# Optimization experiments

Hardware: AMD Instinct MI355X
Metric: run time of the kernel (lower is better)

The kernel has to match this reference:

```python
import jax, jax.numpy as jnp
import numpy as np

B = 4096
N_DENSE = 13
N_SPARSE = 26
VOCAB = 100000
EMB = 8
CIN_SIZE = [26, 128, 128]


def setup_inputs() -> dict:
    key = jax.random.key(0)
    ks = jax.random.split(key, 24)
    s = 0.05
    dense = jax.random.normal(ks[0], (B, N_DENSE), dtype=jnp.float32)
    sparse = jax.random.randint(ks[1], (B, N_SPARSE), 0, VOCAB).astype(jnp.float32)
    inputs = jnp.concatenate([dense, sparse], axis=1)  # [B, 39]
    emb_tables = jax.random.normal(ks[2], (N_SPARSE, VOCAB, EMB), dtype=jnp.float32) * s
    linear_W = jax.random.normal(ks[3], (39, 1), dtype=jnp.float32) * s
    linear_b = jnp.zeros((1,), dtype=jnp.float32)
    # CIN Conv3d weights: kernel (H_prev, H0, 1) with out_channels H_next -> [H_next, H_prev, H0]
    W_cin0 = jax.random.normal(ks[4], (CIN_SIZE[1], CIN_SIZE[0], CIN_SIZE[0]), dtype=jnp.float32) * s
    b_cin0 = jnp.zeros((CIN_SIZE[1],), dtype=jnp.float32)
    W_cin1 = jax.random.normal(ks[5], (CIN_SIZE[2], CIN_SIZE[1], CIN_SIZE[0]), dtype=jnp.float32) * s
    b_cin1 = jnp.zeros((CIN_SIZE[2],), dtype=jnp.float32)
    cin_lin_W = jax.random.normal(ks[6], (256, 1), dtype=jnp.float32) * s
    cin_lin_b = jnp.zeros((1,), dtype=jnp.float32)
    d_W1 = jax.random.normal(ks[7], (221, 256), dtype=jnp.float32) * s
    d_b1 = jnp.zeros((256,), dtype=jnp.float32)
    d_W2 = jax.random.normal(ks[8], (256, 128), dtype=jnp.float32) * s
    d_b2 = jnp.zeros((128,), dtype=jnp.float32)
    d_W3 = jax.random.normal(ks[9], (128, 64), dtype=jnp.float32) * s
    d_b3 = jnp.zeros((64,), dtype=jnp.float32)
    d_W4 = jax.random.normal(ks[10], (64, 1), dtype=jnp.float32) * s
    d_b4 = jnp.zeros((1,), dtype=jnp.float32)
    return dict(inputs=inputs, emb_tables=emb_tables, linear_W=linear_W, linear_b=linear_b,
                W_cin0=W_cin0, b_cin0=b_cin0, W_cin1=W_cin1, b_cin1=b_cin1,
                cin_lin_W=cin_lin_W, cin_lin_b=cin_lin_b,
                d_W1=d_W1, d_b1=d_b1, d_W2=d_W2, d_b2=d_b2,
                d_W3=d_W3, d_b3=d_b3, d_W4=d_W4, d_b4=d_b4)


def reference(inputs, emb_tables, linear_W, linear_b,
              W_cin0, b_cin0, W_cin1, b_cin1, cin_lin_W, cin_lin_b,
              d_W1, d_b1, d_W2, d_b2, d_W3, d_b3, d_W4, d_b4):
    dense_in = inputs[:, :N_DENSE]                       # [B, 13]
    sparse_idx = inputs[:, N_DENSE:].astype(jnp.int32)   # [B, 26]

    # linear part over the raw inputs
    linear_out = inputs @ linear_W + linear_b            # [B, 1]

    # per-field embedding lookup: tables [F, V, E], idx [B, F] -> emb [B, F, E]
    emb = jax.vmap(lambda t, i: t[i], in_axes=(0, 1), out_axes=1)(emb_tables, sparse_idx)

    # CIN: each layer is an outer product over fields followed by a full-extent
    # Conv3d, i.e. X_{l+1}[b,o,k] = sum_{i,j} X_l[b,i,k] * X_0[b,j,k] * W[o,i,j] + b[o]
    X0 = emb
    Xi = emb
    res = []
    for W, b in ((W_cin0, b_cin0), (W_cin1, b_cin1)):
        Xi = jnp.einsum('bik,bjk,oij->bok', Xi, X0, W) + b[None, :, None]
        res.append(Xi)
    cin_feat = jnp.sum(jnp.concatenate(res, axis=1), axis=-1)  # [B, 256]
    cin_out = jax.nn.relu(cin_feat @ cin_lin_W + cin_lin_b)    # [B, 1]

    # dense MLP over [dense | flattened embeddings]
    h = jnp.concatenate([dense_in, emb.reshape(emb.shape[0], -1)], axis=1)  # [B, 221]
    h = jax.nn.relu(h @ d_W1 + d_b1)
    h = jax.nn.relu(h @ d_W2 + d_b2)
    h = jax.nn.relu(h @ d_W3 + d_b3)
    dense_out = jax.nn.relu(h @ d_W4 + d_b4)                   # [B, 1]

    return jax.nn.sigmoid(linear_out + cin_out + dense_out).reshape(-1)  # [B]
```

## Files before the change

kernel.cpp:

```cpp
#include <hip/hip_runtime.h>
#include <math.h>

#define B     4096
#define ND    13
#define NS    26
#define NF    39
#define VOCAB 100000
#define NP    351
#define NPP   360
#define CHP   45
#define GSTR  28
#define RPB   4
#define XSS   212

#define OFF_GST 0
#define OFF_CST 10080
#define OFF_C2J 10088

__global__ __launch_bounds__(256) void k_pre(const float* __restrict__ W0,
                                             const float* __restrict__ W1,
                                             const float* __restrict__ b0,
                                             const float* __restrict__ b1,
                                             const float* __restrict__ clw,
                                             float* __restrict__ Gst,
                                             float* __restrict__ cst,
                                             float* __restrict__ c2j) {
    int blk = blockIdx.x, tid = threadIdx.x;
    if (blk < 26) {
        int j = blk;
        __shared__ float vh[2][128];
        __shared__ float vj[128];
        __shared__ float c2r[2];
        {
            int i = tid & 127, h = tid >> 7;
            const float* wp = W1 + (long)(h * 64) * 3328 + i * 26 + j;
            float acc = 0.f;
#pragma unroll 8
            for (int o = 0; o < 64; o++) acc += clw[128 + h * 64 + o] * wp[o * 3328];
            vh[h][i] = acc;
        }
        __syncthreads();
        if (tid < 128) {
            float vv = vh[0][tid] + vh[1][tid];
            vj[tid] = vv;
            float c = vv * b0[tid];
            for (int off = 32; off; off >>= 1) c += __shfl_down(c, off, 64);
            if ((tid & 63) == 0) c2r[tid >> 6] = c;
        }
        __syncthreads();
        if (tid == 0) c2j[j] = c2r[0] + c2r[1];
        for (int p = tid; p < NPP; p += 256) {
            float g = 0.f;
            if (p < NP) {
                int l = 0, rem = p;
                while (rem >= NS - l) { rem -= NS - l; l++; }
                int m = l + rem;
                float sym = (l != m) ? 1.f : 0.f;
                const float* wa = W0 + l * 26 + m;
                const float* wb = W0 + m * 26 + l;
#pragma unroll 8
                for (int i = 0; i < 128; i++)
                    g += vj[i] * (wa[i * 676] + sym * wb[i * 676]);
            }
            Gst[p * GSTR + j] = g;
        }
    } else if (blk == 26) {
        for (int p = tid; p < NPP; p += 256) {
            float a = 0.f; int lmbits = 0;
            if (p < NP) {
                int l = 0, rem = p;
                while (rem >= NS - l) { rem -= NS - l; l++; }
                int m = l + rem;
                float sym = (l != m) ? 1.f : 0.f;
                const float* wa = W0 + l * 26 + m;
                const float* wb = W0 + m * 26 + l;
#pragma unroll 8
                for (int o = 0; o < 128; o++)
                    a += clw[o] * (wa[o * 676] + sym * wb[o * 676]);
                lmbits = (l << 5) | m;
            }
            Gst[p * GSTR + 26] = a;
            Gst[p * GSTR + 27] = __int_as_float(lmbits);
        }
    } else {
        __shared__ float red[2];
        float c = 0.f;
        if (tid < 128) {
            c = clw[tid] * b0[tid] + clw[128 + tid] * b1[tid];
            for (int off = 32; off; off >>= 1) c += __shfl_down(c, off, 64);
            if ((tid & 63) == 0) red[tid >> 6] = c;
        }
        __syncthreads();
        if (tid == 0) cst[0] = 8.f * (red[0] + red[1]);
    }
}

__global__ __launch_bounds__(256, 4) void k_main(
    const float* __restrict__ inputs, const float* __restrict__ tables,
    const float* __restrict__ lW, const float* __restrict__ lb,
    const float* __restrict__ Gst, const float* __restrict__ c2j,
    const float* __restrict__ cst,
    const float* __restrict__ dW1, const float* __restrict__ db1,
    const float* __restrict__ dW2, const float* __restrict__ db2,
    const float* __restrict__ dW3, const float* __restrict__ db3,
    const float* __restrict__ dW4, const float* __restrict__ db4,
    const float* __restrict__ clb,
    float* __restrict__ out) {
    __shared__ float insf[RPB][40];
    __shared__ float xs[RPB][XSS];
    __shared__ float inT[256][RPB];
    __shared__ float h1T[256][RPB];
    __shared__ float h2T[128][RPB];
    __shared__ float lin_s[RPB], scin_s[RPB];
    __shared__ float redbuf[4][RPB];
    float* inF = &inT[0][0];

    int tid = threadIdx.x;
    int b0r = blockIdx.x * RPB;

    for (int t = tid; t < RPB * NF; t += 256) {
        int r = t / NF, c = t - r * NF;
        insf[r][c] = inputs[(b0r + r) * NF + c];
    }
    __syncthreads();

    if (tid < RPB * NS) {
        int r = tid / NS, f = tid - r * NS;
        int idx = (int)insf[r][ND + f];
        const float4* src = (const float4*)(tables + ((long)f * VOCAB + idx) * 8);
        float4 a = src[0], b4 = src[1];
        float4* dst = (float4*)&xs[r][f * 8];
        dst[0] = a; dst[1] = b4;
        int cb = ND + f * 8;
        inT[cb + 0][r] = a.x;  inT[cb + 1][r] = a.y;
        inT[cb + 2][r] = a.z;  inT[cb + 3][r] = a.w;
        inT[cb + 4][r] = b4.x; inT[cb + 5][r] = b4.y;
        inT[cb + 6][r] = b4.z; inT[cb + 7][r] = b4.w;
    }
    if (tid >= 128 && tid < 128 + RPB * ND) {
        int t = tid - 128;
        int r = t / ND, c = t - r * ND;
        inT[c][r] = insf[r][c];
    }
    if (tid >= 192 && tid < 192 + RPB) {
        int r = tid - 192;
        float acc = lb[0];
        for (int c = 0; c < NF; c++) acc += insf[r][c] * lW[c];
        lin_s[r] = acc;
    }
    __syncthreads();

    {
        int lane = tid & 63, w = tid >> 6;
        int pg = lane >> 5;
        int r = (lane >> 3) & 3;
        int k = lane & 7;
        int chunk = w * 2 + pg;
        const float* xrow = &xs[r][0];
        float t[27];
#pragma unroll
        for (int j = 0; j < 27; j++) t[j] = 0.f;
        const float4* grow = (const float4*)(Gst + chunk * CHP * GSTR);
#pragma unroll 2
        for (int pi = 0; pi < CHP; pi++) {
            float4 g6 = grow[pi * 7 + 6];
            int lm = __float_as_int(g6.w);
            float q = xrow[(lm >> 5) * 8 + k] * xrow[(lm & 31) * 8 + k];
            float4 g0 = grow[pi * 7 + 0], g1 = grow[pi * 7 + 1];
            float4 g2 = grow[pi * 7 + 2], g3 = grow[pi * 7 + 3];
            float4 g4 = grow[pi * 7 + 4], g5 = grow[pi * 7 + 5];
            t[0]  += g0.x * q; t[1]  += g0.y * q; t[2]  += g0.z * q; t[3]  += g0.w * q;
            t[4]  += g1.x * q; t[5]  += g1.y * q; t[6]  += g1.z * q; t[7]  += g1.w * q;
            t[8]  += g2.x * q; t[9]  += g2.y * q; t[10] += g2.z * q; t[11] += g2.w * q;
            t[12] += g3.x * q; t[13] += g3.y * q; t[14] += g3.z * q; t[15] += g3.w * q;
            t[16] += g4.x * q; t[17] += g4.y * q; t[18] += g4.z * q; t[19] += g4.w * q;
            t[20] += g5.x * q; t[21] += g5.y * q; t[22] += g5.z * q; t[23] += g5.w * q;
            t[24] += g6.x * q; t[25] += g6.y * q; t[26] += g6.z * q;
        }
        float csel = (chunk == 0) ? 1.f : 0.f;
        float part = t[26];
#pragma unroll
        for (int j = 0; j < 26; j++) {
            float xv = xrow[j * 8 + k];
            part += (t[j] + csel * c2j[j]) * xv;
        }
        part += __shfl_xor(part, 1, 64);
        part += __shfl_xor(part, 2, 64);
        part += __shfl_xor(part, 4, 64);
        part += __shfl_xor(part, 32, 64);
        if ((lane & 39) == 0) redbuf[w][r] = part;
    }
    __syncthreads();

    if (tid < RPB) {
        float s = cst[0];
        for (int w = 0; w < 4; w++) s += redbuf[w][tid];
        scin_s[tid] = s;
    }
    {
        float bias = db1[tid];
        float a0 = bias, a1 = bias, a2 = bias, a3 = bias;
        for (int c = 0; c < 221; c++) {
            float wv = dW1[c * 256 + tid];
            float4 iv = *(const float4*)&inT[c][0];
            a0 += iv.x * wv; a1 += iv.y * wv; a2 += iv.z * wv; a3 += iv.w * wv;
        }
        float4 o0;
        o0.x = fmaxf(a0, 0.f); o0.y = fmaxf(a1, 0.f);
        o0.z = fmaxf(a2, 0.f); o0.w = fmaxf(a3, 0.f);
        *(float4*)&h1T[tid][0] = o0;
    }
    __syncthreads();

    {
        int o = tid & 127, cg = tid >> 7;
        float bias = (cg == 0) ? db2[o] : 0.f;
        float a0 = bias, a1 = bias, a2 = bias, a3 = bias;
        const float* wbase = dW2 + cg * 128 * 128 + o;
        const float* hbase = &h1T[cg * 128][0];
        for (int c = 0; c < 128; c++) {
            float wv = wbase[c * 128];
            float4 iv = *(const float4*)(hbase + c * RPB);
            a0 += iv.x * wv; a1 += iv.y * wv; a2 += iv.z * wv; a3 += iv.w * wv;
        }
        *(float4*)&inF[tid * 4] = make_float4(a0, a1, a2, a3);
    }
    __syncthreads();
    if (tid < 128) {
        float4 p0 = *(const float4*)&inF[tid * 4];
        float4 p1 = *(const float4*)&inF[(tid + 128) * 4];
        float4 o0;
        o0.x = fmaxf(p0.x + p1.x, 0.f); o0.y = fmaxf(p0.y + p1.y, 0.f);
        o0.z = fmaxf(p0.z + p1.z, 0.f); o0.w = fmaxf(p0.w + p1.w, 0.f);
        *(float4*)&h2T[tid][0] = o0;
    }
    __syncthreads();

    {
        int o = tid & 63, cg = tid >> 6;
        float bias = (cg == 0) ? db3[o] : 0.f;
        float a0 = bias, a1 = bias, a2 = bias, a3 = bias;
        const float* wbase = dW3 + cg * 32 * 64 + o;
        const float* hbase = &h2T[cg * 32][0];
        for (int c = 0; c < 32; c++) {
            float wv = wbase[c * 64];
            float4 iv = *(const float4*)(hbase + c * RPB);
            a0 += iv.x * wv; a1 += iv.y * wv; a2 += iv.z * wv; a3 += iv.w * wv;
        }
        *(float4*)&inF[tid * 4] = make_float4(a0, a1, a2, a3);
    }
    __syncthreads();

    if (tid < 64) {
        float s0 = 0.f, s1 = 0.f, s2 = 0.f, s3 = 0.f;
#pragma unroll
        for (int cg = 0; cg < 4; cg++) {
            float4 pv = *(const float4*)&inF[(cg * 64 + tid) * 4];
            s0 += pv.x; s1 += pv.y; s2 += pv.z; s3 += pv.w;
        }
        float w4 = dW4[tid];
        s0 = fmaxf(s0, 0.f) * w4; s1 = fmaxf(s1, 0.f) * w4;
        s2 = fmaxf(s2, 0.f) * w4; s3 = fmaxf(s3, 0.f) * w4;
#pragma unroll
        for (int off = 1; off < 64; off <<= 1) {
            s0 += __shfl_xor(s0, off, 64);
            s1 += __shfl_xor(s1, off, 64);
            s2 += __shfl_xor(s2, off, 64);
            s3 += __shfl_xor(s3, off, 64);
        }
        if (tid == 0) {
            float sv[4] = { s0, s1, s2, s3 };
            float bb = db4[0], cb = clb[0];
#pragma unroll
            for (int r = 0; r < RPB; r++) {
                float dense = fmaxf(sv[r] + bb, 0.f);
                float cin = fmaxf(scin_s[r] + cb, 0.f);
                float x = lin_s[r] + cin + dense;
                out[b0r + r] = 1.f / (1.f + expf(-x));
            }
        }
    }
}

extern "C" void kernel_launch(void* const* d_in, const int* in_sizes, int n_in,
                              void* d_out, int out_size, void* d_ws, size_t ws_size,
                              hipStream_t stream) {
    const float* inputs = (const float*)d_in[0];
    const float* tables = (const float*)d_in[1];
    const float* lW     = (const float*)d_in[2];
    const float* lb     = (const float*)d_in[3];
    const float* W0     = (const float*)d_in[4];
    const float* b0     = (const float*)d_in[5];
    const float* W1c    = (const float*)d_in[6];
    const float* b1c    = (const float*)d_in[7];
    const float* clw    = (const float*)d_in[8];
    const float* clb    = (const float*)d_in[9];
    const float* dW1    = (const float*)d_in[10];
    const float* db1    = (const float*)d_in[11];
    const float* dW2    = (const float*)d_in[12];
    const float* db2    = (const float*)d_in[13];
    const float* dW3    = (const float*)d_in[14];
    const float* db3    = (const float*)d_in[15];
    const float* dW4    = (const float*)d_in[16];
    const float* db4    = (const float*)d_in[17];

    float* ws   = (float*)d_ws;
    float* Gst  = ws + OFF_GST;
    float* cst  = ws + OFF_CST;
    float* c2j  = ws + OFF_C2J;

    k_pre<<<28, 256, 0, stream>>>(W0, W1c, b0, b1c, clw, Gst, cst, c2j);
    k_main<<<B / RPB, 256, 0, stream>>>(inputs, tables, lW, lb, Gst, c2j, cst,
                                        dW1, db1, dW2, db2, dW3, db3, dW4, db4, clb,
                                        (float*)d_out);
}
```

Before: 227.9 us.

## Process 8 rows per block with 512 threads and split-K MLP layers

Doubles the rows per block from 4 to 8 and the block size to 512 threads, so each weight load of the CIN G-table and the MLP weight matrices is reused across twice as many batch rows. Each wavefront now owns one CIN chunk with a wave-uniform chunk index, which lets the G-table reads become scalar loads. The MLP layers are re-partitioned into split-K groups that reduce through a new shared partial buffer. The cost is more shared memory and registers per block, which may reduce occupancy, and half as many blocks in the grid.

```diff
diff --git a/kernel.cpp b/kernel.cpp
--- a/kernel.cpp
+++ b/kernel.cpp
@@ -10,7 +10,8 @@
 #define NPP   360
 #define CHP   45
 #define GSTR  28
-#define RPB   4
+#define RPB   8
+#define NT    512
 #define XSS   212
 
 #define OFF_GST 0
@@ -95,7 +96,7 @@
     }
 }
 
-__global__ __launch_bounds__(256, 4) void k_main(
+__global__ __launch_bounds__(NT, 4) void k_main(
     const float* __restrict__ inputs, const float* __restrict__ tables,
     const float* __restrict__ lW, const float* __restrict__ lb,
     const float* __restrict__ Gst, const float* __restrict__ c2j,
@@ -111,15 +112,15 @@
     __shared__ float inT[256][RPB];
     __shared__ float h1T[256][RPB];
     __shared__ float h2T[128][RPB];
+    __shared__ float pbuf[NT][RPB];
     __shared__ float lin_s[RPB], scin_s[RPB];
-    __shared__ float redbuf[4][RPB];
-    float* inF = &inT[0][0];
+    __shared__ float redbuf[8][RPB];
 
     int tid = threadIdx.x;
     int b0r = blockIdx.x * RPB;
 
-    for (int t = tid; t < RPB * NF; t += 256) {
-        int r = t / NF, c = t - r * NF;
+    if (tid < RPB * NF) {
+        int r = tid / NF, c = tid - r * NF;
         insf[r][c] = inputs[(b0r + r) * NF + c];
     }
     __syncthreads();
@@ -136,14 +137,12 @@
         inT[cb + 2][r] = a.z;  inT[cb + 3][r] = a.w;
         inT[cb + 4][r] = b4.x; inT[cb + 5][r] = b4.y;
         inT[cb + 6][r] = b4.z; inT[cb + 7][r] = b4.w;
-    }
-    if (tid >= 128 && tid < 128 + RPB * ND) {
-        int t = tid - 128;
+    } else if (tid >= 256 && tid < 256 + RPB * ND) {
+        int t = tid - 256;
         int r = t / ND, c = t - r * ND;
         inT[c][r] = insf[r][c];
-    }
-    if (tid >= 192 && tid < 192 + RPB) {
-        int r = tid - 192;
+    } else if (tid >= 384 && tid < 384 + RPB) {
+        int r = tid - 384;
         float acc = lb[0];
         for (int c = 0; c < NF; c++) acc += insf[r][c] * lW[c];
         lin_s[r] = acc;
@@ -151,64 +150,69 @@
     __syncthreads();
 
     {
-        int lane = tid & 63, w = tid >> 6;
-        int pg = lane >> 5;
-        int r = (lane >> 3) & 3;
-        int k = lane & 7;
-        int chunk = w * 2 + pg;
+        int lane = tid & 63;
+        int w = tid >> 6;
+        int chunk = __builtin_amdgcn_readfirstlane(w);
+        int r = lane >> 3, k = lane & 7;
         const float* xrow = &xs[r][0];
+        const float* gr = Gst + chunk * (CHP * GSTR);
         float t[27];
 #pragma unroll
         for (int j = 0; j < 27; j++) t[j] = 0.f;
-        const float4* grow = (const float4*)(Gst + chunk * CHP * GSTR);
-#pragma unroll 2
         for (int pi = 0; pi < CHP; pi++) {
-            float4 g6 = grow[pi * 7 + 6];
-            int lm = __float_as_int(g6.w);
+            const float* g = gr + pi * GSTR;
+            int lm = __float_as_int(g[27]);
             float q = xrow[(lm >> 5) * 8 + k] * xrow[(lm & 31) * 8 + k];
-            float4 g0 = grow[pi * 7 + 0], g1 = grow[pi * 7 + 1];
-            float4 g2 = grow[pi * 7 + 2], g3 = grow[pi * 7 + 3];
-            float4 g4 = grow[pi * 7 + 4], g5 = grow[pi * 7 + 5];
-            t[0]  += g0.x * q; t[1]  += g0.y * q; t[2]  += g0.z * q; t[3]  += g0.w * q;
-            t[4]  += g1.x * q; t[5]  += g1.y * q; t[6]  += g1.z * q; t[7]  += g1.w * q;
-            t[8]  += g2.x * q; t[9]  += g2.y * q; t[10] += g2.z * q; t[11] += g2.w * q;
-            t[12] += g3.x * q; t[13] += g3.y * q; t[14] += g3.z * q; t[15] += g3.w * q;
-            t[16] += g4.x * q; t[17] += g4.y * q; t[18] += g4.z * q; t[19] += g4.w * q;
-            t[20] += g5.x * q; t[21] += g5.y * q; t[22] += g5.z * q; t[23] += g5.w * q;
-            t[24] += g6.x * q; t[25] += g6.y * q; t[26] += g6.z * q;
+#pragma unroll
+            for (int j = 0; j < 27; j++) t[j] += g[j] * q;
         }
         float csel = (chunk == 0) ? 1.f : 0.f;
         float part = t[26];
 #pragma unroll
-        for (int j = 0; j < 26; j++) {
-            float xv = xrow[j * 8 + k];
-            part += (t[j] + csel * c2j[j]) * xv;
-        }
+        for (int j = 0; j < 26; j++)
+            part += (t[j] + csel * c2j[j]) * xrow[j * 8 + k];
         part += __shfl_xor(part, 1, 64);
         part += __shfl_xor(part, 2, 64);
         part += __shfl_xor(part, 4, 64);
-        part += __shfl_xor(part, 32, 64);
-        if ((lane & 39) == 0) redbuf[w][r] = part;
+        if (k == 0) redbuf[w][r] = part;
     }
     __syncthreads();
 
     if (tid < RPB) {
         float s = cst[0];
-        for (int w = 0; w < 4; w++) s += redbuf[w][tid];
+#pragma unroll
+        for (int w = 0; w < 8; w++) s += redbuf[w][tid];
         scin_s[tid] = s;
     }
     {
-        float bias = db1[tid];
+        int o = tid & 255, cg = tid >> 8;
+        int c0 = cg ? 111 : 0, c1 = cg ? 221 : 111;
+        float bias = cg ? 0.f : db1[o];
         float a0 = bias, a1 = bias, a2 = bias, a3 = bias;
-        for (int c = 0; c < 221; c++) {
-            float wv = dW1[c * 256 + tid];
-            float4 iv = *(const float4*)&inT[c][0];
-            a0 += iv.x * wv; a1 += iv.y * wv; a2 += iv.z * wv; a3 += iv.w * wv;
-        }
-        float4 o0;
-        o0.x = fmaxf(a0, 0.f); o0.y = fmaxf(a1, 0.f);
-        o0.z = fmaxf(a2, 0.f); o0.w = fmaxf(a3, 0.f);
+        float a4 = bias, a5 = bias, a6 = bias, a7 = bias;
+        for (int c = c0; c < c1; c++) {
+            float wv = dW1[c * 256 + o];
+            float4 i0 = *(const float4*)&inT[c][0];
+            float4 i1 = *(const float4*)&inT[c][4];
+            a0 += i0.x * wv; a1 += i0.y * wv; a2 += i0.z * wv; a3 += i0.w * wv;
+            a4 += i1.x * wv; a5 += i1.y * wv; a6 += i1.z * wv; a7 += i1.w * wv;
+        }
+        *(float4*)&pbuf[tid][0] = make_float4(a0, a1, a2, a3);
+        *(float4*)&pbuf[tid][4] = make_float4(a4, a5, a6, a7);
+    }
+    __syncthreads();
+    if (tid < 256) {
+        float4 p0 = *(const float4*)&pbuf[tid][0];
+        float4 p1 = *(const float4*)&pbuf[tid][4];
+        float4 q0 = *(const float4*)&pbuf[tid + 256][0];
+        float4 q1 = *(const float4*)&pbuf[tid + 256][4];
+        float4 o0, o1;
+        o0.x = fmaxf(p0.x + q0.x, 0.f); o0.y = fmaxf(p0.y + q0.y, 0.f);
+        o0.z = fmaxf(p0.z + q0.z, 0.f); o0.w = fmaxf(p0.w + q0.w, 0.f);
+        o1.x = fmaxf(p1.x + q1.x, 0.f); o1.y = fmaxf(p1.y + q1.y, 0.f);
+        o1.z = fmaxf(p1.z + q1.z, 0.f); o1.w = fmaxf(p1.w + q1.w, 0.f);
         *(float4*)&h1T[tid][0] = o0;
+        *(float4*)&h1T[tid][4] = o1;
     }
     __syncthreads();
 
@@ -216,23 +220,38 @@
         int o = tid & 127, cg = tid >> 7;
         float bias = (cg == 0) ? db2[o] : 0.f;
         float a0 = bias, a1 = bias, a2 = bias, a3 = bias;
-        const float* wbase = dW2 + cg * 128 * 128 + o;
-        const float* hbase = &h1T[cg * 128][0];
-        for (int c = 0; c < 128; c++) {
-            float wv = wbase[c * 128];
-            float4 iv = *(const float4*)(hbase + c * RPB);
-            a0 += iv.x * wv; a1 += iv.y * wv; a2 += iv.z * wv; a3 += iv.w * wv;
-        }
-        *(float4*)&inF[tid * 4] = make_float4(a0, a1, a2, a3);
+        float a4 = bias, a5 = bias, a6 = bias, a7 = bias;
+        const float* wb = dW2 + o;
+        for (int cc = 0; cc < 64; cc++) {
+            int c = cg * 64 + cc;
+            float wv = wb[c * 128];
+            float4 i0 = *(const float4*)&h1T[c][0];
+            float4 i1 = *(const float4*)&h1T[c][4];
+            a0 += i0.x * wv; a1 += i0.y * wv; a2 += i0.z * wv; a3 += i0.w * wv;
+            a4 += i1.x * wv; a5 += i1.y * wv; a6 += i1.z * wv; a7 += i1.w * wv;
+        }
+        *(float4*)&pbuf[tid][0] = make_float4(a0, a1, a2, a3);
+        *(float4*)&pbuf[tid][4] = make_float4(a4, a5, a6, a7);
     }
     __syncthreads();
     if (tid < 128) {
-        float4 p0 = *(const float4*)&inF[tid * 4];
-        float4 p1 = *(const float4*)&inF[(tid + 128) * 4];
-        float4 o0;
-        o0.x = fmaxf(p0.x + p1.x, 0.f); o0.y = fmaxf(p0.y + p1.y, 0.f);
-        o0.z = fmaxf(p0.z + p1.z, 0.f); o0.w = fmaxf(p0.w + p1.w, 0.f);
+        float s[8];
+#pragma unroll
+        for (int i = 0; i < 8; i++) s[i] = 0.f;
+#pragma unroll
+        for (int g = 0; g < 4; g++) {
+            float4 p0 = *(const float4*)&pbuf[tid + g * 128][0];
+            float4 p1 = *(const float4*)&pbuf[tid + g * 128][4];
+            s[0] += p0.x; s[1] += p0.y; s[2] += p0.z; s[3] += p0.w;
+            s[4] += p1.x; s[5] += p1.y; s[6] += p1.z; s[7] += p1.w;
+        }
+        float4 o0, o1;
+        o0.x = fmaxf(s[0], 0.f); o0.y = fmaxf(s[1], 0.f);
+        o0.z = fmaxf(s[2], 0.f); o0.w = fmaxf(s[3], 0.f);
+        o1.x = fmaxf(s[4], 0.f); o1.y = fmaxf(s[5], 0.f);
+        o1.z = fmaxf(s[6], 0.f); o1.w = fmaxf(s[7], 0.f);
         *(float4*)&h2T[tid][0] = o0;
+        *(float4*)&h2T[tid][4] = o1;
     }
     __syncthreads();
 
@@ -240,40 +259,44 @@
         int o = tid & 63, cg = tid >> 6;
         float bias = (cg == 0) ? db3[o] : 0.f;
         float a0 = bias, a1 = bias, a2 = bias, a3 = bias;
-        const float* wbase = dW3 + cg * 32 * 64 + o;
-        const float* hbase = &h2T[cg * 32][0];
-        for (int c = 0; c < 32; c++) {
-            float wv = wbase[c * 64];
-            float4 iv = *(const float4*)(hbase + c * RPB);
-            a0 += iv.x * wv; a1 += iv.y * wv; a2 += iv.z * wv; a3 += iv.w * wv;
-        }
-        *(float4*)&inF[tid * 4] = make_float4(a0, a1, a2, a3);
+        float a4 = bias, a5 = bias, a6 = bias, a7 = bias;
+        const float* wb = dW3 + o;
+        for (int cc = 0; cc < 16; cc++) {
+            int c = cg * 16 + cc;
+            float wv = wb[c * 64];
+            float4 i0 = *(const float4*)&h2T[c][0];
+            float4 i1 = *(const float4*)&h2T[c][4];
+            a0 += i0.x * wv; a1 += i0.y * wv; a2 += i0.z * wv; a3 += i0.w * wv;
+            a4 += i1.x * wv; a5 += i1.y * wv; a6 += i1.z * wv; a7 += i1.w * wv;
+        }
+        *(float4*)&pbuf[tid][0] = make_float4(a0, a1, a2, a3);
+        *(float4*)&pbuf[tid][4] = make_float4(a4, a5, a6, a7);
     }
     __syncthreads();
 
     if (tid < 64) {
-        float s0 = 0.f, s1 = 0.f, s2 = 0.f, s3 = 0.f;
-#pragma unroll
-        for (int cg = 0; cg < 4; cg++) {
-            float4 pv = *(const float4*)&inF[(cg * 64 + tid) * 4];
-            s0 += pv.x; s1 += pv.y; s2 += pv.z; s3 += pv.w;
+        float s[8];
+#pragma unroll
+        for (int i = 0; i < 8; i++) s[i] = 0.f;
+#pragma unroll
+        for (int g = 0; g < 8; g++) {
+            float4 p0 = *(const float4*)&pbuf[tid + g * 64][0];
+            float4 p1 = *(const float4*)&pbuf[tid + g * 64][4];
+            s[0] += p0.x; s[1] += p0.y; s[2] += p0.z; s[3] += p0.w;
+            s[4] += p1.x; s[5] += p1.y; s[6] += p1.z; s[7] += p1.w;
         }
         float w4 = dW4[tid];
-        s0 = fmaxf(s0, 0.f) * w4; s1 = fmaxf(s1, 0.f) * w4;
-        s2 = fmaxf(s2, 0.f) * w4; s3 = fmaxf(s3, 0.f) * w4;
-#pragma unroll
-        for (int off = 1; off < 64; off <<= 1) {
-            s0 += __shfl_xor(s0, off, 64);
-            s1 += __shfl_xor(s1, off, 64);
-            s2 += __shfl_xor(s2, off, 64);
-            s3 += __shfl_xor(s3, off, 64);
-        }
+#pragma unroll
+        for (int i = 0; i < 8; i++) s[i] = fmaxf(s[i], 0.f) * w4;
+#pragma unroll
+        for (int off = 1; off < 64; off <<= 1)
+#pragma unroll
+            for (int i = 0; i < 8; i++) s[i] += __shfl_xor(s[i], off, 64);
         if (tid == 0) {
-            float sv[4] = { s0, s1, s2, s3 };
             float bb = db4[0], cb = clb[0];
 #pragma unroll
             for (int r = 0; r < RPB; r++) {
-                float dense = fmaxf(sv[r] + bb, 0.f);
+                float dense = fmaxf(s[r] + bb, 0.f);
                 float cin = fmaxf(scin_s[r] + cb, 0.f);
                 float x = lin_s[r] + cin + dense;
                 out[b0r + r] = 1.f / (1.f + expf(-x));
@@ -310,7 +333,7 @@
     float* c2j  = ws + OFF_C2J;
 
     k_pre<<<28, 256, 0, stream>>>(W0, W1c, b0, b1c, clw, Gst, cst, c2j);
-    k_main<<<B / RPB, 256, 0, stream>>>(inputs, tables, lW, lb, Gst, c2j, cst,
-                                        dW1, db1, dW2, db2, dW3, db3, dW4, db4, clb,
-                                        (float*)d_out);
+    k_main<<<B / RPB, NT, 0, stream>>>(inputs, tables, lW, lb, Gst, c2j, cst,
+                                       dW1, db1, dW2, db2, dW3, db3, dW4, db4, clb,
+                                       (float*)d_out);
 }
```

New measurement: 233.4 us. +2.4%, slower.

## Split fused kernel into per-row CIN kernel and tiled MLP kernels

Applied to the files above, without the earlier changes.

Replaces the single fused per-4-row kernel with three kernels: a 64-thread per-row kernel that gathers embeddings and computes the linear and CIN terms and writes the MLP input to workspace, a first-layer MLP kernel that tiles 16 rows by 64 outputs with a 4-way K split, and a kernel for the remaining MLP layers plus the final sigmoid. The goal is more weight reuse per global load in the 221x256 layer and more parallelism for the CIN stage. In exchange it adds two kernel launches and round-trips activations through global memory.

```diff
diff --git a/kernel.cpp b/kernel.cpp
--- a/kernel.cpp
+++ b/kernel.cpp
@@ -10,12 +10,14 @@
 #define NPP   360
 #define CHP   45
 #define GSTR  28
-#define RPB   4
-#define XSS   212
-
-#define OFF_GST 0
-#define OFF_CST 10080
-#define OFF_C2J 10088
+
+#define OFF_GST  0
+#define OFF_CST  10080
+#define OFF_C2J  10088
+#define OFF_LIN  10240
+#define OFF_SCIN 14336
+#define OFF_H0   18432
+#define OFF_H1   935936
 
 __global__ __launch_bounds__(256) void k_pre(const float* __restrict__ W0,
                                              const float* __restrict__ W1,
@@ -95,172 +97,194 @@
     }
 }
 
-__global__ __launch_bounds__(256, 4) void k_main(
+__global__ __launch_bounds__(64, 4) void k_rows(
     const float* __restrict__ inputs, const float* __restrict__ tables,
     const float* __restrict__ lW, const float* __restrict__ lb,
     const float* __restrict__ Gst, const float* __restrict__ c2j,
     const float* __restrict__ cst,
-    const float* __restrict__ dW1, const float* __restrict__ db1,
-    const float* __restrict__ dW2, const float* __restrict__ db2,
-    const float* __restrict__ dW3, const float* __restrict__ db3,
-    const float* __restrict__ dW4, const float* __restrict__ db4,
-    const float* __restrict__ clb,
-    float* __restrict__ out) {
-    __shared__ float insf[RPB][40];
-    __shared__ float xs[RPB][XSS];
-    __shared__ float inT[256][RPB];
-    __shared__ float h1T[256][RPB];
-    __shared__ float h2T[128][RPB];
-    __shared__ float lin_s[RPB], scin_s[RPB];
-    __shared__ float redbuf[4][RPB];
-    float* inF = &inT[0][0];
-
-    int tid = threadIdx.x;
-    int b0r = blockIdx.x * RPB;
-
-    for (int t = tid; t < RPB * NF; t += 256) {
-        int r = t / NF, c = t - r * NF;
-        insf[r][c] = inputs[(b0r + r) * NF + c];
-    }
-    __syncthreads();
-
-    if (tid < RPB * NS) {
-        int r = tid / NS, f = tid - r * NS;
-        int idx = (int)insf[r][ND + f];
-        const float4* src = (const float4*)(tables + ((long)f * VOCAB + idx) * 8);
-        float4 a = src[0], b4 = src[1];
-        float4* dst = (float4*)&xs[r][f * 8];
-        dst[0] = a; dst[1] = b4;
-        int cb = ND + f * 8;
-        inT[cb + 0][r] = a.x;  inT[cb + 1][r] = a.y;
-        inT[cb + 2][r] = a.z;  inT[cb + 3][r] = a.w;
-        inT[cb + 4][r] = b4.x; inT[cb + 5][r] = b4.y;
-        inT[cb + 6][r] = b4.z; inT[cb + 7][r] = b4.w;
-    }
-    if (tid >= 128 && tid < 128 + RPB * ND) {
-        int t = tid - 128;
-        int r = t / ND, c = t - r * ND;
-        inT[c][r] = insf[r][c];
-    }
-    if (tid >= 192 && tid < 192 + RPB) {
-        int r = tid - 192;
-        float acc = lb[0];
-        for (int c = 0; c < NF; c++) acc += insf[r][c] * lW[c];
-        lin_s[r] = acc;
-    }
-    __syncthreads();
-
+    float* __restrict__ h0, float* __restrict__ lin, float* __restrict__ scin) {
+    __shared__ float insf[40];
+    __shared__ float xs[208];
+    int b = blockIdx.x, lane = threadIdx.x;
+
+    if (lane < NF) insf[lane] = inputs[b * NF + lane];
+    __syncthreads();
+    if (lane < 52) {
+        int f = lane >> 1, h = lane & 1;
+        int idx = (int)insf[ND + f];
+        float4 v = *(const float4*)(tables + ((long)f * VOCAB + idx) * 8 + h * 4);
+        *(float4*)&xs[f * 8 + h * 4] = v;
+    }
+    __syncthreads();
+    for (int t = lane; t < 224; t += 64) {
+        float v = (t < ND) ? insf[t] : ((t < 221) ? xs[t - 13] : 0.f);
+        h0[(long)b * 224 + t] = v;
+    }
     {
-        int lane = tid & 63, w = tid >> 6;
-        int pg = lane >> 5;
-        int r = (lane >> 3) & 3;
-        int k = lane & 7;
-        int chunk = w * 2 + pg;
-        const float* xrow = &xs[r][0];
+        float p = (lane < NF) ? insf[lane] * lW[lane] : 0.f;
+#pragma unroll
+        for (int off = 1; off < 64; off <<= 1) p += __shfl_xor(p, off, 64);
+        if (lane == 0) lin[b] = p + lb[0];
+    }
+    {
+        int k = lane & 7, c = lane >> 3;
+        const float* gr = Gst + c * (CHP * GSTR);
         float t[27];
 #pragma unroll
         for (int j = 0; j < 27; j++) t[j] = 0.f;
-        const float4* grow = (const float4*)(Gst + chunk * CHP * GSTR);
-#pragma unroll 2
         for (int pi = 0; pi < CHP; pi++) {
-            float4 g6 = grow[pi * 7 + 6];
+            const float4* g4 = (const float4*)(gr + pi * GSTR);
+            float4 g6 = g4[6];
             int lm = __float_as_int(g6.w);
-            float q = xrow[(lm >> 5) * 8 + k] * xrow[(lm & 31) * 8 + k];
-            float4 g0 = grow[pi * 7 + 0], g1 = grow[pi * 7 + 1];
-            float4 g2 = grow[pi * 7 + 2], g3 = grow[pi * 7 + 3];
-            float4 g4 = grow[pi * 7 + 4], g5 = grow[pi * 7 + 5];
+            float q = xs[(lm >> 5) * 8 + k] * xs[(lm & 31) * 8 + k];
+            float4 g0 = g4[0], g1 = g4[1], g2 = g4[2];
+            float4 g3 = g4[3], g4v = g4[4], g5 = g4[5];
             t[0]  += g0.x * q; t[1]  += g0.y * q; t[2]  += g0.z * q; t[3]  += g0.w * q;
             t[4]  += g1.x * q; t[5]  += g1.y * q; t[6]  += g1.z * q; t[7]  += g1.w * q;
             t[8]  += g2.x * q; t[9]  += g2.y * q; t[10] += g2.z * q; t[11] += g2.w * q;
             t[12] += g3.x * q; t[13] += g3.y * q; t[14] += g3.z * q; t[15] += g3.w * q;
-            t[16] += g4.x * q; t[17] += g4.y * q; t[18] += g4.z * q; t[19] += g4.w * q;
+            t[16] += g4v.x * q; t[17] += g4v.y * q; t[18] += g4v.z * q; t[19] += g4v.w * q;
             t[20] += g5.x * q; t[21] += g5.y * q; t[22] += g5.z * q; t[23] += g5.w * q;
             t[24] += g6.x * q; t[25] += g6.y * q; t[26] += g6.z * q;
         }
-        float csel = (chunk == 0) ? 1.f : 0.f;
+        float csel = (c == 0) ? 1.f : 0.f;
         float part = t[26];
 #pragma unroll
-        for (int j = 0; j < 26; j++) {
-            float xv = xrow[j * 8 + k];
-            part += (t[j] + csel * c2j[j]) * xv;
-        }
-        part += __shfl_xor(part, 1, 64);
-        part += __shfl_xor(part, 2, 64);
-        part += __shfl_xor(part, 4, 64);
-        part += __shfl_xor(part, 32, 64);
-        if ((lane & 39) == 0) redbuf[w][r] = part;
-    }
-    __syncthreads();
-
-    if (tid < RPB) {
-        float s = cst[0];
-        for (int w = 0; w < 4; w++) s += redbuf[w][tid];
-        scin_s[tid] = s;
-    }
+        for (int j = 0; j < 26; j++)
+            part += (t[j] + csel * c2j[j]) * xs[j * 8 + k];
+#pragma unroll
+        for (int off = 1; off < 64; off <<= 1) part += __shfl_xor(part, off, 64);
+        if (lane == 0) scin[b] = part + cst[0];
+    }
+}
+
+#define ITS 20
+__global__ __launch_bounds__(256, 4) void k_dnn1(
+    const float* __restrict__ h0,
+    const float* __restrict__ dW1, const float* __restrict__ db1,
+    float* __restrict__ h1) {
+    __shared__ float inT[224 * ITS];
+    __shared__ float psum[64 * 64];
+    int tid = threadIdx.x;
+    int m16 = (blockIdx.x >> 2) * 16;
+    int ny = blockIdx.x & 3;
+
+    for (int t = tid; t < 56 * 16; t += 256) {
+        int r = t & 15, c4 = t >> 4;
+        float4 v = *(const float4*)&h0[(long)(m16 + r) * 224 + c4 * 4];
+        inT[(c4 * 4 + 0) * ITS + r] = v.x;
+        inT[(c4 * 4 + 1) * ITS + r] = v.y;
+        inT[(c4 * 4 + 2) * ITS + r] = v.z;
+        inT[(c4 * 4 + 3) * ITS + r] = v.w;
+    }
+    __syncthreads();
+
+    int o = tid & 63, ks = tid >> 6;
+    int og = ny * 64 + o;
+    float a[16];
+#pragma unroll
+    for (int i = 0; i < 16; i++) a[i] = 0.f;
+    int c0 = ks * 56, c1 = c0 + 56;
+    if (c1 > 221) c1 = 221;
+    for (int c = c0; c < c1; c++) {
+        float w = dW1[c * 256 + og];
+        const float* ir = &inT[c * ITS];
+        float4 r0 = *(const float4*)(ir + 0);
+        float4 r1 = *(const float4*)(ir + 4);
+        float4 r2 = *(const float4*)(ir + 8);
+        float4 r3 = *(const float4*)(ir + 12);
+        a[0] += r0.x * w; a[1] += r0.y * w; a[2]  += r0.z * w; a[3]  += r0.w * w;
+        a[4] += r1.x * w; a[5] += r1.y * w; a[6]  += r1.z * w; a[7]  += r1.w * w;
+        a[8] += r2.x * w; a[9] += r2.y * w; a[10] += r2.z * w; a[11] += r2.w * w;
+        a[12] += r3.x * w; a[13] += r3.y * w; a[14] += r3.z * w; a[15] += r3.w * w;
+    }
+#pragma unroll
+    for (int r = 0; r < 16; r++) psum[(ks * 16 + r) * 64 + o] = a[r];
+    __syncthreads();
+
+    for (int t = tid; t < 1024; t += 256) {
+        int oi = t & 63, r = t >> 6;
+        float s = psum[(0 * 16 + r) * 64 + oi] + psum[(1 * 16 + r) * 64 + oi]
+                + psum[(2 * 16 + r) * 64 + oi] + psum[(3 * 16 + r) * 64 + oi];
+        s = fmaxf(s + db1[ny * 64 + oi], 0.f);
+        h1[(long)(m16 + r) * 256 + ny * 64 + oi] = s;
+    }
+}
+
+__global__ __launch_bounds__(256, 4) void k_dnnrest(
+    const float* __restrict__ h1,
+    const float* __restrict__ dW2, const float* __restrict__ db2,
+    const float* __restrict__ dW3, const float* __restrict__ db3,
+    const float* __restrict__ dW4, const float* __restrict__ db4,
+    const float* __restrict__ lin, const float* __restrict__ scin,
+    const float* __restrict__ clb,
+    float* __restrict__ out) {
+    __shared__ float h1T[256 * 4];
+    __shared__ float ps[512 * 4];
+    __shared__ float h2T[128 * 4];
+    __shared__ float h3T[64 * 4];
+    int tid = threadIdx.x;
+    int b4 = blockIdx.x * 4;
+
+    for (int t = tid; t < 1024; t += 256) {
+        int c = t & 255, r = t >> 8;
+        h1T[c * 4 + r] = h1[(long)(b4 + r) * 256 + c];
+    }
+    __syncthreads();
     {
-        float bias = db1[tid];
-        float a0 = bias, a1 = bias, a2 = bias, a3 = bias;
-        for (int c = 0; c < 221; c++) {
-            float wv = dW1[c * 256 + tid];
-            float4 iv = *(const float4*)&inT[c][0];
-            a0 += iv.x * wv; a1 += iv.y * wv; a2 += iv.z * wv; a3 += iv.w * wv;
-        }
+        int o = tid & 127, ks = tid >> 7;
+        float a0 = 0.f, a1 = 0.f, a2 = 0.f, a3 = 0.f;
+        for (int c = 0; c < 128; c++) {
+            int cc = ks * 128 + c;
+            float w = dW2[cc * 128 + o];
+            float4 hv = *(const float4*)&h1T[cc * 4];
+            a0 += hv.x * w; a1 += hv.y * w; a2 += hv.z * w; a3 += hv.w * w;
+        }
+        *(float4*)&ps[(ks * 128 + o) * 4] = make_float4(a0, a1, a2, a3);
+    }
+    __syncthreads();
+    if (tid < 128) {
+        float4 p0 = *(const float4*)&ps[tid * 4];
+        float4 p1 = *(const float4*)&ps[(128 + tid) * 4];
+        float bias = db2[tid];
         float4 o0;
-        o0.x = fmaxf(a0, 0.f); o0.y = fmaxf(a1, 0.f);
-        o0.z = fmaxf(a2, 0.f); o0.w = fmaxf(a3, 0.f);
-        *(float4*)&h1T[tid][0] = o0;
-    }
-    __syncthreads();
-
+        o0.x = fmaxf(p0.x + p1.x + bias, 0.f);
+        o0.y = fmaxf(p0.y + p1.y + bias, 0.f);
+        o0.z = fmaxf(p0.z + p1.z + bias, 0.f);
+        o0.w = fmaxf(p0.w + p1.w + bias, 0.f);
+        *(float4*)&h2T[tid * 4] = o0;
+    }
+    __syncthreads();
     {
-        int o = tid & 127, cg = tid >> 7;
-        float bias = (cg == 0) ? db2[o] : 0.f;
-        float a0 = bias, a1 = bias, a2 = bias, a3 = bias;
-        const float* wbase = dW2 + cg * 128 * 128 + o;
-        const float* hbase = &h1T[cg * 128][0];
-        for (int c = 0; c < 128; c++) {
-            float wv = wbase[c * 128];
-            float4 iv = *(const float4*)(hbase + c * RPB);
-            a0 += iv.x * wv; a1 += iv.y * wv; a2 += iv.z * wv; a3 += iv.w * wv;
-        }
-        *(float4*)&inF[tid * 4] = make_float4(a0, a1, a2, a3);
-    }
-    __syncthreads();
-    if (tid < 128) {
-        float4 p0 = *(const float4*)&inF[tid * 4];
-        float4 p1 = *(const float4*)&inF[(tid + 128) * 4];
-        float4 o0;
-        o0.x = fmaxf(p0.x + p1.x, 0.f); o0.y = fmaxf(p0.y + p1.y, 0.f);
-        o0.z = fmaxf(p0.z + p1.z, 0.f); o0.w = fmaxf(p0.w + p1.w, 0.f);
-        *(float4*)&h2T[tid][0] = o0;
-    }
-    __syncthreads();
-
-    {
-        int o = tid & 63, cg = tid >> 6;
-        float bias = (cg == 0) ? db3[o] : 0.f;
-        float a0 = bias, a1 = bias, a2 = bias, a3 = bias;
-        const float* wbase = dW3 + cg * 32 * 64 + o;
-        const float* hbase = &h2T[cg * 32][0];
+        int o = tid & 63, ks = tid >> 6;
+        float a0 = 0.f, a1 = 0.f, a2 = 0.f, a3 = 0.f;
         for (int c = 0; c < 32; c++) {
-            float wv = wbase[c * 64];
-            float4 iv = *(const float4*)(hbase + c * RPB);
-            a0 += iv.x * wv; a1 += iv.y * wv; a2 += iv.z * wv; a3 += iv.w * wv;
-        }
-        *(float4*)&inF[tid * 4] = make_float4(a0, a1, a2, a3);
-    }
-    __syncthreads();
-
+            int cc = ks * 32 + c;
+            float w = dW3[cc * 64 + o];
+            float4 hv = *(const float4*)&h2T[cc * 4];
+            a0 += hv.x * w; a1 += hv.y * w; a2 += hv.z * w; a3 += hv.w * w;
+        }
+        *(float4*)&ps[(ks * 64 + o) * 4] = make_float4(a0, a1, a2, a3);
+    }
+    __syncthreads();
     if (tid < 64) {
         float s0 = 0.f, s1 = 0.f, s2 = 0.f, s3 = 0.f;
 #pragma unroll
-        for (int cg = 0; cg < 4; cg++) {
-            float4 pv = *(const float4*)&inF[(cg * 64 + tid) * 4];
-            s0 += pv.x; s1 += pv.y; s2 += pv.z; s3 += pv.w;
-        }
+        for (int ks = 0; ks < 4; ks++) {
+            float4 p = *(const float4*)&ps[(ks * 64 + tid) * 4];
+            s0 += p.x; s1 += p.y; s2 += p.z; s3 += p.w;
+        }
+        float bias = db3[tid];
+        float4 o0;
+        o0.x = fmaxf(s0 + bias, 0.f); o0.y = fmaxf(s1 + bias, 0.f);
+        o0.z = fmaxf(s2 + bias, 0.f); o0.w = fmaxf(s3 + bias, 0.f);
+        *(float4*)&h3T[tid * 4] = o0;
+    }
+    __syncthreads();
+    if (tid < 64) {
         float w4 = dW4[tid];
-        s0 = fmaxf(s0, 0.f) * w4; s1 = fmaxf(s1, 0.f) * w4;
-        s2 = fmaxf(s2, 0.f) * w4; s3 = fmaxf(s3, 0.f) * w4;
+        float4 h = *(const float4*)&h3T[tid * 4];
+        float s0 = h.x * w4, s1 = h.y * w4, s2 = h.z * w4, s3 = h.w * w4;
 #pragma unroll
         for (int off = 1; off < 64; off <<= 1) {
             s0 += __shfl_xor(s0, off, 64);
@@ -272,11 +296,11 @@
             float sv[4] = { s0, s1, s2, s3 };
             float bb = db4[0], cb = clb[0];
 #pragma unroll
-            for (int r = 0; r < RPB; r++) {
+            for (int r = 0; r < 4; r++) {
                 float dense = fmaxf(sv[r] + bb, 0.f);
-                float cin = fmaxf(scin_s[r] + cb, 0.f);
-                float x = lin_s[r] + cin + dense;
-                out[b0r + r] = 1.f / (1.f + expf(-x));
+                float cin = fmaxf(scin[b4 + r] + cb, 0.f);
+                float x = lin[b4 + r] + cin + dense;
+                out[b4 + r] = 1.f / (1.f + expf(-x));
             }
         }
     }
@@ -308,9 +332,14 @@
     float* Gst  = ws + OFF_GST;
     float* cst  = ws + OFF_CST;
     float* c2j  = ws + OFF_C2J;
+    float* lin  = ws + OFF_LIN;
+    float* scin = ws + OFF_SCIN;
+    float* h0   = ws + OFF_H0;
+    float* h1   = ws + OFF_H1;
 
     k_pre<<<28, 256, 0, stream>>>(W0, W1c, b0, b1c, clw, Gst, cst, c2j);
-    k_main<<<B / RPB, 256, 0, stream>>>(inputs, tables, lW, lb, Gst, c2j, cst,
-                                        dW1, db1, dW2, db2, dW3, db3, dW4, db4, clb,
-                                        (float*)d_out);
-}
+    k_rows<<<B, 64, 0, stream>>>(inputs, tables, lW, lb, Gst, c2j, cst, h0, lin, scin);
+    k_dnn1<<<1024, 256, 0, stream>>>(h0, dW1, db1, h1);
+    k_dnnrest<<<1024, 256, 0, stream>>>(h1, dW2, db2, dW3, db3, dW4, db4,
+                                        lin, scin, clb, (float*)d_out);
+}
```

Result: slower. 246.0 us (+8.0%).

## Halve rows per block and split CIN pair work into sixteen chunks

Applied to the files above, without the earlier changes.

Cuts rows per block from four to two, which doubles the grid to 2048 blocks. The CIN pair loop is repartitioned into 16 chunks of 23 pairs instead of 8 of 45, so each wave covers four chunks for two rows. The MLP stages now use two-row float2 accumulation with separate partial-sum buffers and bias applied at reduction, and the occupancy hint rises to 6. The aim is more parallelism and shorter per-thread serial loops, at the cost of reading the MLP weights from global memory twice as many times overall.

```diff
diff --git a/kernel.cpp b/kernel.cpp
--- a/kernel.cpp
+++ b/kernel.cpp
@@ -7,15 +7,17 @@
 #define NF    39
 #define VOCAB 100000
 #define NP    351
-#define NPP   360
-#define CHP   45
+#define NCH   16
+#define CHP   23
+#define NPP   368
 #define GSTR  28
-#define RPB   4
+#define RPB   2
+#define NT    256
 #define XSS   212
 
 #define OFF_GST 0
-#define OFF_CST 10080
-#define OFF_C2J 10088
+#define OFF_CST 10304
+#define OFF_C2J 10312
 
 __global__ __launch_bounds__(256) void k_pre(const float* __restrict__ W0,
                                              const float* __restrict__ W1,
@@ -95,7 +97,7 @@
     }
 }
 
-__global__ __launch_bounds__(256, 4) void k_main(
+__global__ __launch_bounds__(NT, 6) void k_main(
     const float* __restrict__ inputs, const float* __restrict__ tables,
     const float* __restrict__ lW, const float* __restrict__ lb,
     const float* __restrict__ Gst, const float* __restrict__ c2j,
@@ -108,41 +110,37 @@
     float* __restrict__ out) {
     __shared__ float insf[RPB][40];
     __shared__ float xs[RPB][XSS];
-    __shared__ float inT[256][RPB];
+    __shared__ float inT[224][RPB];
     __shared__ float h1T[256][RPB];
     __shared__ float h2T[128][RPB];
+    __shared__ float h3T[64][RPB];
+    __shared__ float ps[256][RPB];
     __shared__ float lin_s[RPB], scin_s[RPB];
     __shared__ float redbuf[4][RPB];
-    float* inF = &inT[0][0];
 
     int tid = threadIdx.x;
     int b0r = blockIdx.x * RPB;
 
-    for (int t = tid; t < RPB * NF; t += 256) {
-        int r = t / NF, c = t - r * NF;
+    if (tid < RPB * NF) {
+        int r = tid / NF, c = tid - r * NF;
         insf[r][c] = inputs[(b0r + r) * NF + c];
     }
     __syncthreads();
 
-    if (tid < RPB * NS) {
-        int r = tid / NS, f = tid - r * NS;
+    if (tid < RPB * NS * 2) {
+        int t = tid >> 1, h = tid & 1;
+        int r = t / NS, f = t - r * NS;
         int idx = (int)insf[r][ND + f];
-        const float4* src = (const float4*)(tables + ((long)f * VOCAB + idx) * 8);
-        float4 a = src[0], b4 = src[1];
-        float4* dst = (float4*)&xs[r][f * 8];
-        dst[0] = a; dst[1] = b4;
-        int cb = ND + f * 8;
-        inT[cb + 0][r] = a.x;  inT[cb + 1][r] = a.y;
-        inT[cb + 2][r] = a.z;  inT[cb + 3][r] = a.w;
-        inT[cb + 4][r] = b4.x; inT[cb + 5][r] = b4.y;
-        inT[cb + 6][r] = b4.z; inT[cb + 7][r] = b4.w;
-    }
-    if (tid >= 128 && tid < 128 + RPB * ND) {
+        float4 v = *(const float4*)(tables + ((long)f * VOCAB + idx) * 8 + h * 4);
+        *(float4*)&xs[r][f * 8 + h * 4] = v;
+        int cb = ND + f * 8 + h * 4;
+        inT[cb + 0][r] = v.x; inT[cb + 1][r] = v.y;
+        inT[cb + 2][r] = v.z; inT[cb + 3][r] = v.w;
+    } else if (tid >= 128 && tid < 128 + RPB * ND) {
         int t = tid - 128;
         int r = t / ND, c = t - r * ND;
         inT[c][r] = insf[r][c];
-    }
-    if (tid >= 192 && tid < 192 + RPB) {
+    } else if (tid >= 192 && tid < 192 + RPB) {
         int r = tid - 192;
         float acc = lb[0];
         for (int c = 0; c < NF; c++) acc += insf[r][c] * lW[c];
@@ -152,124 +150,123 @@
 
     {
         int lane = tid & 63, w = tid >> 6;
-        int pg = lane >> 5;
-        int r = (lane >> 3) & 3;
-        int k = lane & 7;
-        int chunk = w * 2 + pg;
+        int k = lane & 7, r = (lane >> 3) & 1, cg = lane >> 4;
+        int chunk = w * 4 + cg;
+        const float* gr = Gst + chunk * (CHP * GSTR);
         const float* xrow = &xs[r][0];
         float t[27];
 #pragma unroll
         for (int j = 0; j < 27; j++) t[j] = 0.f;
-        const float4* grow = (const float4*)(Gst + chunk * CHP * GSTR);
-#pragma unroll 2
         for (int pi = 0; pi < CHP; pi++) {
-            float4 g6 = grow[pi * 7 + 6];
+            const float4* g4 = (const float4*)(gr + pi * GSTR);
+            float4 g6 = g4[6];
             int lm = __float_as_int(g6.w);
             float q = xrow[(lm >> 5) * 8 + k] * xrow[(lm & 31) * 8 + k];
-            float4 g0 = grow[pi * 7 + 0], g1 = grow[pi * 7 + 1];
-            float4 g2 = grow[pi * 7 + 2], g3 = grow[pi * 7 + 3];
-            float4 g4 = grow[pi * 7 + 4], g5 = grow[pi * 7 + 5];
-            t[0]  += g0.x * q; t[1]  += g0.y * q; t[2]  += g0.z * q; t[3]  += g0.w * q;
-            t[4]  += g1.x * q; t[5]  += g1.y * q; t[6]  += g1.z * q; t[7]  += g1.w * q;
-            t[8]  += g2.x * q; t[9]  += g2.y * q; t[10] += g2.z * q; t[11] += g2.w * q;
-            t[12] += g3.x * q; t[13] += g3.y * q; t[14] += g3.z * q; t[15] += g3.w * q;
-            t[16] += g4.x * q; t[17] += g4.y * q; t[18] += g4.z * q; t[19] += g4.w * q;
-            t[20] += g5.x * q; t[21] += g5.y * q; t[22] += g5.z * q; t[23] += g5.w * q;
-            t[24] += g6.x * q; t[25] += g6.y * q; t[26] += g6.z * q;
+            float4 g0 = g4[0], g1 = g4[1], g2 = g4[2];
+            float4 g3 = g4[3], g4v = g4[4], g5 = g4[5];
+            t[0]  += g0.x * q;  t[1]  += g0.y * q;  t[2]  += g0.z * q;  t[3]  += g0.w * q;
+            t[4]  += g1.x * q;  t[5]  += g1.y * q;  t[6]  += g1.z * q;  t[7]  += g1.w * q;
+            t[8]  += g2.x * q;  t[9]  += g2.y * q;  t[10] += g2.z * q;  t[11] += g2.w * q;
+            t[12] += g3.x * q;  t[13] += g3.y * q;  t[14] += g3.z * q;  t[15] += g3.w * q;
+            t[16] += g4v.x * q; t[17] += g4v.y * q; t[18] += g4v.z * q; t[19] += g4v.w * q;
+            t[20] += g5.x * q;  t[21] += g5.y * q;  t[22] += g5.z * q;  t[23] += g5.w * q;
+            t[24] += g6.x * q;  t[25] += g6.y * q;  t[26] += g6.z * q;
         }
         float csel = (chunk == 0) ? 1.f : 0.f;
         float part = t[26];
 #pragma unroll
-        for (int j = 0; j < 26; j++) {
-            float xv = xrow[j * 8 + k];
-            part += (t[j] + csel * c2j[j]) * xv;
-        }
+        for (int j = 0; j < 26; j++)
+            part += (t[j] + csel * c2j[j]) * xrow[j * 8 + k];
         part += __shfl_xor(part, 1, 64);
         part += __shfl_xor(part, 2, 64);
         part += __shfl_xor(part, 4, 64);
+        part += __shfl_xor(part, 16, 64);
         part += __shfl_xor(part, 32, 64);
-        if ((lane & 39) == 0) redbuf[w][r] = part;
+        if ((lane & 55) == 0) redbuf[w][r] = part;
     }
     __syncthreads();
 
     if (tid < RPB) {
         float s = cst[0];
+#pragma unroll
         for (int w = 0; w < 4; w++) s += redbuf[w][tid];
         scin_s[tid] = s;
     }
     {
         float bias = db1[tid];
-        float a0 = bias, a1 = bias, a2 = bias, a3 = bias;
+        float a0 = bias, a1 = bias;
+#pragma unroll 4
         for (int c = 0; c < 221; c++) {
-            float wv = dW1[c * 256 + tid];
-            float4 iv = *(const float4*)&inT[c][0];
-            a0 += iv.x * wv; a1 += iv.y * wv; a2 += iv.z * wv; a3 += iv.w * wv;
-        }
-        float4 o0;
-        o0.x = fmaxf(a0, 0.f); o0.y = fmaxf(a1, 0.f);
-        o0.z = fmaxf(a2, 0.f); o0.w = fmaxf(a3, 0.f);
-        *(float4*)&h1T[tid][0] = o0;
+            float w = dW1[c * 256 + tid];
+            float2 iv = *(const float2*)&inT[c][0];
+            a0 += iv.x * w; a1 += iv.y * w;
+        }
+        h1T[tid][0] = fmaxf(a0, 0.f);
+        h1T[tid][1] = fmaxf(a1, 0.f);
     }
     __syncthreads();
 
     {
-        int o = tid & 127, cg = tid >> 7;
-        float bias = (cg == 0) ? db2[o] : 0.f;
-        float a0 = bias, a1 = bias, a2 = bias, a3 = bias;
-        const float* wbase = dW2 + cg * 128 * 128 + o;
-        const float* hbase = &h1T[cg * 128][0];
-        for (int c = 0; c < 128; c++) {
-            float wv = wbase[c * 128];
-            float4 iv = *(const float4*)(hbase + c * RPB);
-            a0 += iv.x * wv; a1 += iv.y * wv; a2 += iv.z * wv; a3 += iv.w * wv;
-        }
-        *(float4*)&inF[tid * 4] = make_float4(a0, a1, a2, a3);
+        int o = tid & 127, ks = tid >> 7;
+        float a0 = 0.f, a1 = 0.f;
+        const float* wb = dW2 + o;
+#pragma unroll 4
+        for (int cc = 0; cc < 128; cc++) {
+            int c = ks * 128 + cc;
+            float w = wb[c * 128];
+            float2 iv = *(const float2*)&h1T[c][0];
+            a0 += iv.x * w; a1 += iv.y * w;
+        }
+        ps[ks * 128 + o][0] = a0;
+        ps[ks * 128 + o][1] = a1;
     }
     __syncthreads();
     if (tid < 128) {
-        float4 p0 = *(const float4*)&inF[tid * 4];
-        float4 p1 = *(const float4*)&inF[(tid + 128) * 4];
-        float4 o0;
-        o0.x = fmaxf(p0.x + p1.x, 0.f); o0.y = fmaxf(p0.y + p1.y, 0.f);
-        o0.z = fmaxf(p0.z + p1.z, 0.f); o0.w = fmaxf(p0.w + p1.w, 0.f);
-        *(float4*)&h2T[tid][0] = o0;
+        float bias = db2[tid];
+        h2T[tid][0] = fmaxf(ps[tid][0] + ps[128 + tid][0] + bias, 0.f);
+        h2T[tid][1] = fmaxf(ps[tid][1] + ps[128 + tid][1] + bias, 0.f);
     }
     __syncthreads();
 
     {
-        int o = tid & 63, cg = tid >> 6;
-        float bias = (cg == 0) ? db3[o] : 0.f;
-        float a0 = bias, a1 = bias, a2 = bias, a3 = bias;
-        const float* wbase = dW3 + cg * 32 * 64 + o;
-        const float* hbase = &h2T[cg * 32][0];
-        for (int c = 0; c < 32; c++) {
-            float wv = wbase[c * 64];
-            float4 iv = *(const float4*)(hbase + c * RPB);
-            a0 += iv.x * wv; a1 += iv.y * wv; a2 += iv.z * wv; a3 += iv.w * wv;
-        }
-        *(float4*)&inF[tid * 4] = make_float4(a0, a1, a2, a3);
-    }
-    __syncthreads();
-
+        int o = tid & 63, ks = tid >> 6;
+        float a0 = 0.f, a1 = 0.f;
+        const float* wb = dW3 + o;
+#pragma unroll 4
+        for (int cc = 0; cc < 32; cc++) {
+            int c = ks * 32 + cc;
+            float w = wb[c * 64];
+            float2 iv = *(const float2*)&h2T[c][0];
+            a0 += iv.x * w; a1 += iv.y * w;
+        }
+        ps[ks * 64 + o][0] = a0;
+        ps[ks * 64 + o][1] = a1;
+    }
+    __syncthreads();
     if (tid < 64) {
-        float s0 = 0.f, s1 = 0.f, s2 = 0.f, s3 = 0.f;
-#pragma unroll
-        for (int cg = 0; cg < 4; cg++) {
-            float4 pv = *(const float4*)&inF[(cg * 64 + tid) * 4];
-            s0 += pv.x; s1 += pv.y; s2 += pv.z; s3 += pv.w;
-        }
+        float s0 = 0.f, s1 = 0.f;
+#pragma unroll
+        for (int ks = 0; ks < 4; ks++) {
+            s0 += ps[ks * 64 + tid][0];
+            s1 += ps[ks * 64 + tid][1];
+        }
+        float bias = db3[tid];
+        h3T[tid][0] = fmaxf(s0 + bias, 0.f);
+        h3T[tid][1] = fmaxf(s1 + bias, 0.f);
+    }
+    __syncthreads();
+
+    if (tid < 64) {
         float w4 = dW4[tid];
-        s0 = fmaxf(s0, 0.f) * w4; s1 = fmaxf(s1, 0.f) * w4;
-        s2 = fmaxf(s2, 0.f) * w4; s3 = fmaxf(s3, 0.f) * w4;
+        float s0 = h3T[tid][0] * w4;
+        float s1 = h3T[tid][1] * w4;
 #pragma unroll
         for (int off = 1; off < 64; off <<= 1) {
             s0 += __shfl_xor(s0, off, 64);
             s1 += __shfl_xor(s1, off, 64);
-            s2 += __shfl_xor(s2, off, 64);
-            s3 += __shfl_xor(s3, off, 64);
         }
         if (tid == 0) {
-            float sv[4] = { s0, s1, s2, s3 };
+            float sv[RPB] = { s0, s1 };
             float bb = db4[0], cb = clb[0];
 #pragma unroll
             for (int r = 0; r < RPB; r++) {
@@ -310,7 +307,7 @@
     float* c2j  = ws + OFF_C2J;
 
     k_pre<<<28, 256, 0, stream>>>(W0, W1c, b0, b1c, clw, Gst, cst, c2j);
-    k_main<<<B / RPB, 256, 0, stream>>>(inputs, tables, lW, lb, Gst, c2j, cst,
-                                        dW1, db1, dW2, db2, dW3, db3, dW4, db4, clb,
-                                        (float*)d_out);
+    k_main<<<B / RPB, NT, 0, stream>>>(inputs, tables, lW, lb, Gst, c2j, cst,
+                                       dW1, db1, dW2, db2, dW3, db3, dW4, db4, clb,
+                                       (float*)d_out);
 }
```

New measurement: 295.3 us. 1.3x slower.
